# Optimization experiments

Measured on AMD Instinct MI355X. Metric: run time of the kernel, lower is better.

## Reference

```python
import jax, jax.numpy as jnp
import numpy as np

B, SK, SQ, H, D, N = 4, 4096, 4096, 16, 64, 32


def setup_inputs() -> dict:
    key = jax.random.key(0)
    k1, k2, k3, k4, k5 = jax.random.split(key, 5)
    return {
        "key_in": jax.random.normal(k1, (B, SK, H), jnp.float32),
        "value": jax.random.normal(k2, (B, SK, H * D), jnp.float32),
        "query": jax.random.normal(k3, (B, SQ, H), jnp.float32),
        "real_amps": jax.random.normal(k4, (H, 1, 1, N), jnp.float32),
        "imag_amps": jax.random.normal(k5, (H, 1, 1, N), jnp.float32) * 0.1,
    }


def reference(key_in, value, query, real_amps, imag_amps):
    h, n = real_amps.shape[0], real_amps.shape[-1]
    b, sk, _ = key_in.shape
    sq = query.shape[1]
    d = value.shape[-1] // h
    # non-trainable freqs buffer: N points in [0, 1] scaled by N*pi
    freqs = (jnp.arange(n, dtype=key_in.dtype) / (n - 1)) * n * jnp.pi  # (N,)
    # reshape to per-head layout: scalar feature per head for q/k
    q = jnp.transpose(query, (2, 0, 1))[..., None]   # (h, b, sq, 1)
    k = jnp.transpose(key_in, (2, 0, 1))[..., None]  # (h, b, sk, 1)
    v = jnp.transpose(value.reshape(b, sk, h, d), (2, 0, 1, 3))  # (h, b, sk, d)
    qp = freqs * q  # (h, b, sq, N)
    kp = freqs * k  # (h, b, sk, N)
    sin_q, cos_q = jnp.sin(qp), jnp.cos(qp)
    sin_k, cos_k = jnp.sin(kp), jnp.cos(kp)
    # trig feature maps, width 4N
    trig_q = jnp.concatenate(
        [real_amps * cos_q, real_amps * sin_q, imag_amps * sin_q, -imag_amps * cos_q],
        axis=-1,
    )  # (h, b, sq, 4N)
    trig_k = jnp.concatenate([cos_k, sin_k, cos_k, sin_k], axis=-1)  # (h, b, sk, 4N)
    # linear attention: (K^T V) then Q (K^T V)
    kv = jnp.einsum('hbkf,hbkd->hbfd', trig_k, v)        # (h, b, 4N, d)
    out = jnp.einsum('hbqf,hbfd->hbqd', trig_q, kv)       # (h, b, sq, d)
    return jnp.transpose(out, (1, 2, 0, 3)).reshape(b, sq, h * d)
```

## Files before the change

### kernel.cpp

```cpp
#include <hip/hip_runtime.h>
#include <math.h>

#define SK 4096
#define SQ 4096
#define HH 16
#define DD 64
#define NN 32

typedef __attribute__((ext_vector_type(8))) short short8;
typedef __attribute__((ext_vector_type(4))) float floatx4;

__device__ __forceinline__ float freq_of(int n) {
    return (float)n * (32.0f * (float)M_PI / 31.0f);
}

__device__ __forceinline__ unsigned short f2bf(float x) {
    unsigned u = __float_as_uint(x);
    u += 0x7FFFu + ((u >> 16) & 1u);
    return (unsigned short)(u >> 16);
}

__device__ __forceinline__ void async16(const float* g, float* l) {
    __builtin_amdgcn_global_load_lds(
        (const __attribute__((address_space(1))) unsigned int*)g,
        (__attribute__((address_space(3))) unsigned int*)l, 16, 0, 0);
}

template <int NC>
__global__ __launch_bounds__(256) void k1_partial(
    const float* __restrict__ key_in, const float* __restrict__ value,
    float* __restrict__ P)
{
    constexpr int KPC = SK / NC;
    constexpr int NB  = KPC / 64;
    const int chunk = blockIdx.x & (NC - 1);
    const int bh    = blockIdx.x / NC;
    const int b = bh >> 4, h = bh & 15;
    const int tid = threadIdx.x;
    const int w = tid >> 6, l = tid & 63;

    __shared__ float vt[2][64 * DD];
    __shared__ float kt[KPC];

    const int k0 = chunk * KPC;

    auto issue = [&](int bb, int p) {
        const int kb = k0 + bb * 64;
        #pragma unroll
        for (int i = 0; i < 4; ++i) {
            const float* gv = value
                + (size_t)(b * SK + kb + (w * 4 + i) * 4 + (l >> 4)) * (HH * DD)
                + h * DD + (l & 15) * 4;
            async16(gv, &vt[p][(w * 4 + i) * 256]);
        }
    };

    issue(0, 0);
    #pragma unroll
    for (int i = 0; i < KPC / 256; ++i)
        kt[tid + i * 256] = key_in[(size_t)(b * SK + k0 + tid + i * 256) * HH + h];

    const int fl = l & 15;
    const int qd = l >> 4;
    const int feat = w * 16 + fl;
    const float fn = freq_of(feat & 31);
    const bool use_sin = (w >= 2);

    floatx4 acc[4];
    #pragma unroll
    for (int dt = 0; dt < 4; ++dt) acc[dt] = (floatx4){0.f, 0.f, 0.f, 0.f};

    for (int bb = 0; bb < NB; ++bb) {
        const int p = bb & 1;
        __syncthreads();
        if (bb + 1 < NB) issue(bb + 1, p ^ 1);

        #pragma unroll
        for (int s = 0; s < 2; ++s) {
            const int kk = bb * 64 + s * 32 + qd * 8;
            float4 ka  = *(const float4*)&kt[kk];
            float4 kb4 = *(const float4*)&kt[kk + 4];
            float kj[8] = {ka.x, ka.y, ka.z, ka.w, kb4.x, kb4.y, kb4.z, kb4.w};

            union { short8 v; unsigned short u[8]; } A;
            #pragma unroll
            for (int j = 0; j < 8; ++j) {
                float ang = fn * kj[j];
                A.u[j] = f2bf(use_sin ? __sinf(ang) : __cosf(ang));
            }

            const int vb = (s * 32 + qd * 8) * DD + fl;
            #pragma unroll
            for (int dt = 0; dt < 4; ++dt) {
                union { short8 v; unsigned short u[8]; } Bf;
                #pragma unroll
                for (int j = 0; j < 8; ++j)
                    Bf.u[j] = f2bf(vt[p][vb + j * DD + dt * 16]);
                acc[dt] = __builtin_amdgcn_mfma_f32_16x16x32_bf16(
                    A.v, Bf.v, acc[dt], 0, 0, 0);
            }
        }
    }

    float* Pb = P + ((size_t)chunk * 64 + bh) * (2 * NN * DD);
    #pragma unroll
    for (int dt = 0; dt < 4; ++dt)
        #pragma unroll
        for (int r = 0; r < 4; ++r) {
            int frow = w * 16 + qd * 4 + r;
            Pb[frow * DD + dt * 16 + fl] = acc[dt][r];
        }
}

template <int NC>
__global__ __launch_bounds__(256) void k1_reduce(
    const float* __restrict__ P, float* __restrict__ CS)
{
    int gid = blockIdx.x * 256 + threadIdx.x;
    float acc = 0.f;
    #pragma unroll
    for (int c = 0; c < NC; ++c)
        acc += P[(size_t)c * (64 * 2 * NN * DD) + gid];
    CS[gid] = acc;
}

__global__ __launch_bounds__(256) void k2_out(
    const float* __restrict__ query, const float* __restrict__ ramps,
    const float* __restrict__ iamps, const float* __restrict__ CS,
    float* __restrict__ out)
{
    const int bh = blockIdx.x >> 6;
    const int qc = blockIdx.x & 63;
    const int b = bh >> 4, h = bh & 15;
    const int qbase = qc * 64;
    const int tid = threadIdx.x;
    const int w = tid >> 6, l = tid & 63;

    __shared__ unsigned short cst[64 * 64];
    __shared__ float qv[64];

    {
        const float* CSb = CS + (size_t)bh * (2 * NN * DD);
        const int feat = tid >> 2, dbase = (tid & 3) * 16;
        const int fb = feat >> 3, f7 = feat & 7;
        #pragma unroll
        for (int i = 0; i < 4; ++i) {
            float4 v = *(const float4*)&CSb[feat * DD + dbase + i * 4];
            float vv[4] = {v.x, v.y, v.z, v.w};
            #pragma unroll
            for (int e = 0; e < 4; ++e) {
                int d = dbase + i * 4 + e;
                cst[d * 64 + ((fb ^ (d & 7)) << 3) + f7] = f2bf(vv[e]);
            }
        }
    }
    if (tid < 64)
        qv[tid] = query[(size_t)(b * SQ + qbase + tid) * HH + h];
    __syncthreads();

    const int fl = l & 15, qd = l >> 4;
    const float qval = qv[w * 16 + fl];
    const int nb = qd * 8;
    float4 raA = *(const float4*)&ramps[h * NN + nb];
    float4 raB = *(const float4*)&ramps[h * NN + nb + 4];
    float4 iaA = *(const float4*)&iamps[h * NN + nb];
    float4 iaB = *(const float4*)&iamps[h * NN + nb + 4];
    float ra[8] = {raA.x, raA.y, raA.z, raA.w, raB.x, raB.y, raB.z, raB.w};
    float ia[8] = {iaA.x, iaA.y, iaA.z, iaA.w, iaB.x, iaB.y, iaB.z, iaB.w};

    union { short8 v; unsigned short u[8]; } A0, A1;
    #pragma unroll
    for (int j = 0; j < 8; ++j) {
        float s, c;
        __sincosf(freq_of(nb + j) * qval, &s, &c);
        A0.u[j] = f2bf(ra[j] * c + ia[j] * s);
        A1.u[j] = f2bf(ra[j] * s - ia[j] * c);
    }

    floatx4 acc[4];
    #pragma unroll
    for (int dt = 0; dt < 4; ++dt) acc[dt] = (floatx4){0.f, 0.f, 0.f, 0.f};

    #pragma unroll
    for (int dt = 0; dt < 4; ++dt) {
        const int d = dt * 16 + fl;
        short8 B0 = *(const short8*)&cst[d * 64 + ((qd ^ (d & 7)) << 3)];
        short8 B1 = *(const short8*)&cst[d * 64 + (((4 + qd) ^ (d & 7)) << 3)];
        acc[dt] = __builtin_amdgcn_mfma_f32_16x16x32_bf16(A0.v, B0, acc[dt], 0, 0, 0);
        acc[dt] = __builtin_amdgcn_mfma_f32_16x16x32_bf16(A1.v, B1, acc[dt], 0, 0, 0);
    }

    float* ob = out + ((size_t)(b * SQ + qbase) * HH + h) * DD;
    #pragma unroll
    for (int dt = 0; dt < 4; ++dt)
        #pragma unroll
        for (int r = 0; r < 4; ++r) {
            int q = w * 16 + qd * 4 + r;
            ob[(size_t)q * (HH * DD) + dt * 16 + fl] = acc[dt][r];
        }
}

extern "C" void kernel_launch(void* const* d_in, const int* in_sizes, int n_in,
                              void* d_out, int out_size, void* d_ws, size_t ws_size,
                              hipStream_t stream) {
    const float* key_in = (const float*)d_in[0];
    const float* value  = (const float*)d_in[1];
    const float* query  = (const float*)d_in[2];
    const float* ramps  = (const float*)d_in[3];
    const float* iamps  = (const float*)d_in[4];
    float* out = (float*)d_out;

    const size_t CS_FLOATS  = 64 * 2 * NN * DD;
    const size_t P16_FLOATS = (size_t)16 * CS_FLOATS;
    const size_t need16 = (P16_FLOATS + CS_FLOATS) * sizeof(float);

    float* P = (float*)d_ws;

    if (ws_size >= need16) {
        float* CSp = P + P16_FLOATS;
        hipLaunchKernelGGL((k1_partial<16>), dim3(64 * 16), dim3(256), 0, stream,
                           key_in, value, P);
        hipLaunchKernelGGL((k1_reduce<16>), dim3(CS_FLOATS / 256), dim3(256), 0, stream,
                           P, CSp);
        hipLaunchKernelGGL(k2_out, dim3(64 * 64), dim3(256), 0, stream,
                           query, ramps, iamps, CSp, out);
    } else {
        float* CSp = P + (size_t)8 * CS_FLOATS;
        hipLaunchKernelGGL((k1_partial<8>), dim3(64 * 8), dim3(256), 0, stream,
                           key_in, value, P);
        hipLaunchKernelGGL((k1_reduce<8>), dim3(CS_FLOATS / 256), dim3(256), 0, stream,
                           P, CSp);
        hipLaunchKernelGGL(k2_out, dim3(64 * 64), dim3(256), 0, stream,
                           query, ramps, iamps, CSp, out);
    }
}
```

Measured before the change: 138.8 us.

## Pre-convert value tiles to bf16 in LDS, vectorize reduce, double q per block

The value tile in k1_partial is now loaded into registers, converted once to bf16 and stored to LDS in a swizzled K-contiguous layout, so each MFMA B operand is a single 16-byte LDS read. This replaces the async global-to-LDS fp32 copy plus per-element strided reads and repeated conversion. The key lookup is permuted to match the new k ordering. k1_reduce now uses float4 loads, and k2_out handles 128 queries per block so the bf16 CS tile staging is amortized over twice the work. The trade-off is losing the async LDS copy overlap and using more registers.

New measurement: 136.1 us. 2.0% less time.

```diff
diff --git a/kernel.cpp b/kernel.cpp
--- a/kernel.cpp
+++ b/kernel.cpp
@@ -9,6 +9,7 @@
 
 typedef __attribute__((ext_vector_type(8))) short short8;
 typedef __attribute__((ext_vector_type(4))) float floatx4;
+typedef __attribute__((ext_vector_type(4))) unsigned short us4;
 
 __device__ __forceinline__ float freq_of(int n) {
     return (float)n * (32.0f * (float)M_PI / 31.0f);
@@ -18,12 +19,6 @@
     unsigned u = __float_as_uint(x);
     u += 0x7FFFu + ((u >> 16) & 1u);
     return (unsigned short)(u >> 16);
-}
-
-__device__ __forceinline__ void async16(const float* g, float* l) {
-    __builtin_amdgcn_global_load_lds(
-        (const __attribute__((address_space(1))) unsigned int*)g,
-        (__attribute__((address_space(3))) unsigned int*)l, 16, 0, 0);
 }
 
 template <int NC>
@@ -39,23 +34,13 @@
     const int tid = threadIdx.x;
     const int w = tid >> 6, l = tid & 63;
 
-    __shared__ float vt[2][64 * DD];
+    __shared__ unsigned short vtb[2][64 * 64];
     __shared__ float kt[KPC];
 
     const int k0 = chunk * KPC;
-
-    auto issue = [&](int bb, int p) {
-        const int kb = k0 + bb * 64;
-        #pragma unroll
-        for (int i = 0; i < 4; ++i) {
-            const float* gv = value
-                + (size_t)(b * SK + kb + (w * 4 + i) * 4 + (l >> 4)) * (HH * DD)
-                + h * DD + (l & 15) * 4;
-            async16(gv, &vt[p][(w * 4 + i) * 256]);
-        }
-    };
-
-    issue(0, 0);
+    const int g  = tid & 15;
+    const int kq = tid >> 4;
+
     #pragma unroll
     for (int i = 0; i < KPC / 256; ++i)
         kt[tid + i * 256] = key_in[(size_t)(b * SK + k0 + tid + i * 256) * HH + h];
@@ -70,17 +55,46 @@
     #pragma unroll
     for (int dt = 0; dt < 4; ++dt) acc[dt] = (floatx4){0.f, 0.f, 0.f, 0.f};
 
+    union F4 { float4 v; float f[4]; };
+    F4 L[2][4];
+
+    auto vload = [&](int bb, int p) {
+        const int kb = k0 + bb * 64;
+        #pragma unroll
+        for (int jj = 0; jj < 4; ++jj)
+            L[p][jj].v = *(const float4*)(value
+                + (size_t)(b * SK + kb + jj * 16 + kq) * (HH * DD) + h * DD + g * 4);
+    };
+
+    auto vstore = [&](int p) {
+        #pragma unroll
+        for (int e = 0; e < 4; ++e) {
+            const int d = g * 4 + e;
+            union { us4 v; unsigned short u[4]; } px;
+            #pragma unroll
+            for (int jj = 0; jj < 4; ++jj)
+                px.u[jj] = f2bf(L[p][jj].f[e]);
+            *(us4*)&vtb[p][d * 64 + ((((kq >> 1) ^ (d & 7)) << 3) | ((kq & 1) << 2))]
+                = px.v;
+        }
+    };
+
+    vload(0, 0);
+    #pragma unroll
     for (int bb = 0; bb < NB; ++bb) {
         const int p = bb & 1;
+        if (bb + 1 < NB) vload(bb + 1, p ^ 1);
+        vstore(p);
         __syncthreads();
-        if (bb + 1 < NB) issue(bb + 1, p ^ 1);
 
         #pragma unroll
         for (int s = 0; s < 2; ++s) {
-            const int kk = bb * 64 + s * 32 + qd * 8;
-            float4 ka  = *(const float4*)&kt[kk];
-            float4 kb4 = *(const float4*)&kt[kk + 4];
-            float kj[8] = {ka.x, ka.y, ka.z, ka.w, kb4.x, kb4.y, kb4.z, kb4.w};
+            const int cb = bb * 64 + s * 8 + qd * 2;
+            float2 p0 = *(const float2*)&kt[cb];
+            float2 p1 = *(const float2*)&kt[cb + 16];
+            float2 p2 = *(const float2*)&kt[cb + 32];
+            float2 p3 = *(const float2*)&kt[cb + 48];
+            float kj[8] = {p0.x, p1.x, p2.x, p3.x, p0.y, p1.y, p2.y, p3.y};
 
             union { short8 v; unsigned short u[8]; } A;
             #pragma unroll
@@ -89,15 +103,13 @@
                 A.u[j] = f2bf(use_sin ? __sinf(ang) : __cosf(ang));
             }
 
-            const int vb = (s * 32 + qd * 8) * DD + fl;
             #pragma unroll
             for (int dt = 0; dt < 4; ++dt) {
-                union { short8 v; unsigned short u[8]; } Bf;
-                #pragma unroll
-                for (int j = 0; j < 8; ++j)
-                    Bf.u[j] = f2bf(vt[p][vb + j * DD + dt * 16]);
+                const int d = dt * 16 + fl;
+                short8 B = *(const short8*)
+                    &vtb[p][d * 64 + ((((s << 2) | qd) ^ (d & 7)) << 3)];
                 acc[dt] = __builtin_amdgcn_mfma_f32_16x16x32_bf16(
-                    A.v, Bf.v, acc[dt], 0, 0, 0);
+                    A.v, B, acc[dt], 0, 0, 0);
             }
         }
     }
@@ -116,12 +128,14 @@
 __global__ __launch_bounds__(256) void k1_reduce(
     const float* __restrict__ P, float* __restrict__ CS)
 {
-    int gid = blockIdx.x * 256 + threadIdx.x;
-    float acc = 0.f;
-    #pragma unroll
-    for (int c = 0; c < NC; ++c)
-        acc += P[(size_t)c * (64 * 2 * NN * DD) + gid];
-    CS[gid] = acc;
+    int gid = (blockIdx.x * 256 + threadIdx.x) * 4;
+    float4 a = {0.f, 0.f, 0.f, 0.f};
+    #pragma unroll
+    for (int c = 0; c < NC; ++c) {
+        float4 v = *(const float4*)&P[(size_t)c * (64 * 2 * NN * DD) + gid];
+        a.x += v.x; a.y += v.y; a.z += v.z; a.w += v.w;
+    }
+    *(float4*)&CS[gid] = a;
 }
 
 __global__ __launch_bounds__(256) void k2_out(
@@ -129,15 +143,15 @@
     const float* __restrict__ iamps, const float* __restrict__ CS,
     float* __restrict__ out)
 {
-    const int bh = blockIdx.x >> 6;
-    const int qc = blockIdx.x & 63;
+    const int bh = blockIdx.x >> 5;
+    const int qc = blockIdx.x & 31;
     const int b = bh >> 4, h = bh & 15;
-    const int qbase = qc * 64;
+    const int qbase = qc * 128;
     const int tid = threadIdx.x;
     const int w = tid >> 6, l = tid & 63;
 
     __shared__ unsigned short cst[64 * 64];
-    __shared__ float qv[64];
+    __shared__ float qv[128];
 
     {
         const float* CSb = CS + (size_t)bh * (2 * NN * DD);
@@ -154,12 +168,11 @@
             }
         }
     }
-    if (tid < 64)
+    if (tid < 128)
         qv[tid] = query[(size_t)(b * SQ + qbase + tid) * HH + h];
     __syncthreads();
 
     const int fl = l & 15, qd = l >> 4;
-    const float qval = qv[w * 16 + fl];
     const int nb = qd * 8;
     float4 raA = *(const float4*)&ramps[h * NN + nb];
     float4 raB = *(const float4*)&ramps[h * NN + nb + 4];
@@ -168,36 +181,50 @@
     float ra[8] = {raA.x, raA.y, raA.z, raA.w, raB.x, raB.y, raB.z, raB.w};
     float ia[8] = {iaA.x, iaA.y, iaA.z, iaA.w, iaB.x, iaB.y, iaB.z, iaB.w};
 
-    union { short8 v; unsigned short u[8]; } A0, A1;
-    #pragma unroll
-    for (int j = 0; j < 8; ++j) {
-        float s, c;
-        __sincosf(freq_of(nb + j) * qval, &s, &c);
-        A0.u[j] = f2bf(ra[j] * c + ia[j] * s);
-        A1.u[j] = f2bf(ra[j] * s - ia[j] * c);
-    }
-
-    floatx4 acc[4];
-    #pragma unroll
-    for (int dt = 0; dt < 4; ++dt) acc[dt] = (floatx4){0.f, 0.f, 0.f, 0.f};
+    union AB { short8 v; unsigned short u[8]; };
+    AB A0[2], A1[2];
+    #pragma unroll
+    for (int hh = 0; hh < 2; ++hh) {
+        const float qval = qv[hh * 64 + w * 16 + fl];
+        #pragma unroll
+        for (int j = 0; j < 8; ++j) {
+            float s, c;
+            __sincosf(freq_of(nb + j) * qval, &s, &c);
+            A0[hh].u[j] = f2bf(ra[j] * c + ia[j] * s);
+            A1[hh].u[j] = f2bf(ra[j] * s - ia[j] * c);
+        }
+    }
+
+    floatx4 acc[2][4];
+    #pragma unroll
+    for (int hh = 0; hh < 2; ++hh)
+        #pragma unroll
+        for (int dt = 0; dt < 4; ++dt) acc[hh][dt] = (floatx4){0.f, 0.f, 0.f, 0.f};
 
     #pragma unroll
     for (int dt = 0; dt < 4; ++dt) {
         const int d = dt * 16 + fl;
         short8 B0 = *(const short8*)&cst[d * 64 + ((qd ^ (d & 7)) << 3)];
         short8 B1 = *(const short8*)&cst[d * 64 + (((4 + qd) ^ (d & 7)) << 3)];
-        acc[dt] = __builtin_amdgcn_mfma_f32_16x16x32_bf16(A0.v, B0, acc[dt], 0, 0, 0);
-        acc[dt] = __builtin_amdgcn_mfma_f32_16x16x32_bf16(A1.v, B1, acc[dt], 0, 0, 0);
+        #pragma unroll
+        for (int hh = 0; hh < 2; ++hh) {
+            acc[hh][dt] = __builtin_amdgcn_mfma_f32_16x16x32_bf16(
+                A0[hh].v, B0, acc[hh][dt], 0, 0, 0);
+            acc[hh][dt] = __builtin_amdgcn_mfma_f32_16x16x32_bf16(
+                A1[hh].v, B1, acc[hh][dt], 0, 0, 0);
+        }
     }
 
     float* ob = out + ((size_t)(b * SQ + qbase) * HH + h) * DD;
     #pragma unroll
-    for (int dt = 0; dt < 4; ++dt)
-        #pragma unroll
-        for (int r = 0; r < 4; ++r) {
-            int q = w * 16 + qd * 4 + r;
-            ob[(size_t)q * (HH * DD) + dt * 16 + fl] = acc[dt][r];
-        }
+    for (int hh = 0; hh < 2; ++hh)
+        #pragma unroll
+        for (int dt = 0; dt < 4; ++dt)
+            #pragma unroll
+            for (int r = 0; r < 4; ++r) {
+                int q = hh * 64 + w * 16 + qd * 4 + r;
+                ob[(size_t)q * (HH * DD) + dt * 16 + fl] = acc[hh][dt][r];
+            }
 }
 
 extern "C" void kernel_launch(void* const* d_in, const int* in_sizes, int n_in,
@@ -220,17 +247,17 @@
         float* CSp = P + P16_FLOATS;
         hipLaunchKernelGGL((k1_partial<16>), dim3(64 * 16), dim3(256), 0, stream,
                            key_in, value, P);
-        hipLaunchKernelGGL((k1_reduce<16>), dim3(CS_FLOATS / 256), dim3(256), 0, stream,
+        hipLaunchKernelGGL((k1_reduce<16>), dim3(CS_FLOATS / 1024), dim3(256), 0, stream,
                            P, CSp);
-        hipLaunchKernelGGL(k2_out, dim3(64 * 64), dim3(256), 0, stream,
+        hipLaunchKernelGGL(k2_out, dim3(64 * 32), dim3(256), 0, stream,
                            query, ramps, iamps, CSp, out);
     } else {
         float* CSp = P + (size_t)8 * CS_FLOATS;
         hipLaunchKernelGGL((k1_partial<8>), dim3(64 * 8), dim3(256), 0, stream,
                            key_in, value, P);
-        hipLaunchKernelGGL((k1_reduce<8>), dim3(CS_FLOATS / 256), dim3(256), 0, stream,
+        hipLaunchKernelGGL((k1_reduce<8>), dim3(CS_FLOATS / 1024), dim3(256), 0, stream,
                            P, CSp);
-        hipLaunchKernelGGL(k2_out, dim3(64 * 64), dim3(256), 0, stream,
+        hipLaunchKernelGGL(k2_out, dim3(64 * 32), dim3(256), 0, stream,
                            query, ramps, iamps, CSp, out);
     }
 }
```
